# Optimization experiments

Measured on AMD Instinct MI355X. Metric: run time of the kernel, lower is better.

## Reference

```python
import jax, jax.numpy as jnp
import numpy as np

KS = 3          # deform conv kernel size
PAD = 1         # zero padding
NUM_HEADS = 6
DIM = 192


def conv2d(x, w, b=None, stride=1, padding=0):
    out = jax.lax.conv_general_dilated(
        x, w, (stride, stride), [(padding, padding), (padding, padding)],
        dimension_numbers=('NCHW', 'OIHW', 'NCHW'))
    if b is not None:
        out = out + b[None, :, None, None]
    return out


def deform_conv(x, p_conv_w, p_conv_b, dconv_w):
    B, C, H, W = x.shape
    N = KS * KS
    offset = conv2d(x, p_conv_w, p_conv_b, padding=1)           # [B, 2N, H, W]
    xp = jnp.pad(x, ((0, 0), (0, 0), (PAD, PAD), (PAD, PAD)))   # zero pad
    Hp, Wp = H + 2 * PAD, W + 2 * PAD
    # kernel-relative offsets p_n, row-major, first N are x (rows), last N are y (cols)
    r = jnp.arange(-(KS - 1) // 2, (KS - 1) // 2 + 1, dtype=x.dtype)
    pnx, pny = jnp.meshgrid(r, r, indexing='ij')
    p_n = jnp.concatenate([pnx.ravel(), pny.ravel()])           # [2N]
    # base grid p_0 (coords in padded image, starting at 1)
    p0x, p0y = jnp.meshgrid(jnp.arange(1, H + 1, dtype=x.dtype),
                            jnp.arange(1, W + 1, dtype=x.dtype), indexing='ij')
    p0 = jnp.concatenate([jnp.tile(p0x[None], (N, 1, 1)),
                          jnp.tile(p0y[None], (N, 1, 1))], axis=0)  # [2N,H,W]
    p = p0[None] + p_n[None, :, None, None] + offset            # [B,2N,H,W]
    p = jnp.transpose(p, (0, 2, 3, 1))                          # [B,H,W,2N]
    px, py = p[..., :N], p[..., N:]
    fx = jnp.floor(jax.lax.stop_gradient(px))                   # .detach().floor()
    fy = jnp.floor(jax.lax.stop_gradient(py))
    qx0 = jnp.clip(fx, 0, Hp - 1).astype(jnp.int32)
    qy0 = jnp.clip(fy, 0, Wp - 1).astype(jnp.int32)
    qx1 = jnp.clip(fx + 1, 0, Hp - 1).astype(jnp.int32)
    qy1 = jnp.clip(fy + 1, 0, Wp - 1).astype(jnp.int32)
    pxc = jnp.clip(px, 0, Hp - 1)
    pyc = jnp.clip(py, 0, Wp - 1)
    g_lt = (1 + (qx0 - pxc)) * (1 + (qy0 - pyc))
    g_rb = (1 - (qx1 - pxc)) * (1 - (qy1 - pyc))
    g_lb = (1 + (qx0 - pxc)) * (1 - (qy1 - pyc))
    g_rt = (1 - (qx1 - pxc)) * (1 + (qy0 - pyc))
    xf = xp.reshape(B, C, Hp * Wp)

    def gather(qx, qy):
        idx = (qx * Wp + qy).reshape(B, 1, -1)                  # [B,1,H*W*N]
        return jnp.take_along_axis(xf, idx, axis=-1).reshape(B, C, H, W, N)

    x_off = (g_lt[:, None] * gather(qx0, qy0)
             + g_rb[:, None] * gather(qx1, qy1)
             + g_lb[:, None] * gather(qx0, qy1)
             + g_rt[:, None] * gather(qx1, qy0))                # [B,C,H,W,N]
    # _reshape_x_offset: out[h*ks+r, w*ks+c] = x_off[h,w,r*ks+c]
    x_big = x_off.reshape(B, C, H, W, KS, KS)
    x_big = jnp.transpose(x_big, (0, 1, 2, 4, 3, 5)).reshape(B, C, H * KS, W * KS)
    return conv2d(x_big, dconv_w, stride=KS)                    # [B,C,H,W], no bias


def _l2_normalize(t):
    n = jnp.sqrt(jnp.sum(t * t, axis=-1, keepdims=True))
    return t / jnp.maximum(n, 1e-12)


def setup_inputs() -> dict:
    key = jax.random.key(0)
    ks = jax.random.split(key, 6)
    B, C, H, W = 2, DIM, 96, 96
    return {
        'x': jax.random.normal(ks[0], (B, C, H, W), dtype=jnp.float32),
        'p_conv_w': jax.random.normal(ks[1], (2 * KS * KS, C, 3, 3), dtype=jnp.float32) * 0.01,
        'p_conv_b': jax.random.normal(ks[2], (2 * KS * KS,), dtype=jnp.float32) * 0.01,
        'dconv_w': jax.random.normal(ks[3], (C, C, KS, KS), dtype=jnp.float32) * 0.02,
        'qkv_w': jax.random.normal(ks[4], (3 * C, C), dtype=jnp.float32) * 0.05,
        'proj_w': jax.random.normal(ks[5], (C, C), dtype=jnp.float32) * 0.05,
        'temperature': jnp.ones((NUM_HEADS, 1, 1), dtype=jnp.float32),
    }


def reference(x, p_conv_w, p_conv_b, dconv_w, qkv_w, proj_w, temperature):
    B, C, H, W = x.shape
    q = deform_conv(x, p_conv_w, p_conv_b, dconv_w)             # [B,C,H,W]
    qkv = jnp.einsum('bchw,oc->bohw', x, qkv_w)                 # 1x1 conv, no bias
    k, v = qkv[:, C:2 * C], qkv[:, 2 * C:]                      # q from qkv discarded
    hd = C // NUM_HEADS
    qh = _l2_normalize(q.reshape(B, NUM_HEADS, hd, H * W))
    kh = _l2_normalize(k.reshape(B, NUM_HEADS, hd, H * W))
    vh = v.reshape(B, NUM_HEADS, hd, H * W)
    attn = jnp.einsum('bhcn,bhdn->bhcd', qh, kh) * temperature[None]
    attn = jax.nn.softmax(attn, axis=-1)
    out = jnp.einsum('bhcd,bhdn->bhcn', attn, vh).reshape(B, C, H, W)
    return jnp.einsum('bchw,oc->bohw', out, proj_w)             # 1x1 project_out
```

## Files before the change

### kernel.cpp

```cpp
#include <hip/hip_runtime.h>

constexpr int SPLITS = 24;
constexpr size_t OFF_OFS  = 0;
constexpr size_t Q_OFS    = 331776;
constexpr size_t K_OFS    = Q_OFS + 3538944;
constexpr size_t V_OFS    = K_OFS + 3538944;
constexpr size_t NQ_OFS   = V_OFS + 3538944;
constexpr size_t NK_OFS   = NQ_OFS + 384;
constexpr size_t PART_OFS = NK_OFS + 384;
constexpr size_t ATTN_OFS = PART_OFS + (size_t)SPLITS * 12 * 1024;
constexpr size_t W2_OFS   = ATTN_OFS + 12288;
constexpr size_t XOFF_OFS = 11330304;
constexpr size_t WBT_OFS  = XOFF_OFS + 7962624;

typedef __attribute__((ext_vector_type(8))) short bf16x8;
typedef __attribute__((ext_vector_type(4))) float f32x4;

__device__ __forceinline__ unsigned bf16rne(float f) {
  unsigned u = __float_as_uint(f);
  return (u + 0x7fffu + ((u >> 16) & 1u)) >> 16;
}

__global__ __launch_bounds__(192) void k_offc_part(
    const float* __restrict__ x, const float* __restrict__ pw,
    float* __restrict__ part)
{
  __shared__ float band[16 * 4 * 98];
  int blk = blockIdx.x;
  int csp = blk % 12;
  int rem = blk / 12;
  int b  = rem / 48;
  int r0 = (rem % 48) * 2;
  int c0 = csp * 16;
  int t  = threadIdx.x;
  int r = t / 96, w = t % 96;

  for (int i = 0; i < 33; ++i) {
    int e = t + i * 192;
    if (e < 6272) {
      int cc = e / 392, r2 = e % 392;
      int row = r2 / 98, col = r2 % 98;
      int gr = r0 + row - 1, gc = col - 1;
      float v = 0.f;
      if (gr >= 0 && gr < 96 && gc >= 0 && gc < 96)
        v = x[((b * 192 + c0 + cc) * 96 + gr) * 96 + gc];
      band[cc * 392 + row * 98 + col] = v;
    }
  }
  __syncthreads();

  float acc[18] = {};
#pragma unroll 4
  for (int cc = 0; cc < 16; ++cc) {
    float bv[9];
#pragma unroll
    for (int ki = 0; ki < 3; ++ki)
#pragma unroll
      for (int kj = 0; kj < 3; ++kj)
        bv[ki * 3 + kj] = band[cc * 392 + (r + ki) * 98 + w + kj];
#pragma unroll
    for (int o = 0; o < 18; ++o) {
      float w9[9];
#pragma unroll
      for (int kk = 0; kk < 9; ++kk)
        w9[kk] = pw[(o * 192 + c0 + cc) * 9 + kk];
#pragma unroll
      for (int kk = 0; kk < 9; ++kk)
        acc[o] += w9[kk] * bv[kk];
    }
  }
  float* dst = &part[(size_t)csp * 663552 + ((size_t)(b * 18) * 96 + r0 + r) * 96 + w];
#pragma unroll
  for (int o = 0; o < 18; ++o)
    dst[(size_t)o * 9216] = acc[o];
}

__global__ __launch_bounds__(256) void k_offc_red(
    const float4* __restrict__ part4, const float* __restrict__ pb,
    float4* __restrict__ off4)
{
  int i4 = blockIdx.x * 256 + threadIdx.x;
  if (i4 >= 165888) return;
  int o = ((i4 * 4) / 9216) % 18;
  float bb = pb[o];
  float4 s = {bb, bb, bb, bb};
  for (int sp = 0; sp < 12; ++sp) {
    float4 v = part4[(size_t)sp * 165888 + i4];
    s.x += v.x; s.y += v.y; s.z += v.z; s.w += v.w;
  }
  off4[i4] = s;
}

__global__ __launch_bounds__(256) void k_cvtw(
    const float4* __restrict__ dw4, uint2* __restrict__ out, int n4)
{
  int i = blockIdx.x * 256 + threadIdx.x;
  if (i < n4) {
    float4 v = dw4[i];
    out[i] = uint2{bf16rne(v.x) | (bf16rne(v.y) << 16),
                   bf16rne(v.z) | (bf16rne(v.w) << 16)};
  }
}

__global__ __launch_bounds__(256) void k_sample(
    const float* __restrict__ x, const float* __restrict__ off,
    unsigned* __restrict__ xoffu, int b)
{
  __shared__ float twt[4][288];
  __shared__ int   tof[4][288];
  int blk = blockIdx.x;
  int csp = blk & 3;
  int tile = blk >> 2;
  int h  = tile / 3;
  int w0 = (tile % 3) * 32;
  int t  = threadIdx.x;

  for (int e = t; e < 288; e += 256) {
    int n = e >> 5, pix = e & 31;
    int ki = n / 3, kj = n % 3;
    int w = w0 + pix;
    float ox = off[((b * 18 + n) * 96 + h) * 96 + w];
    float oy = off[((b * 18 + 9 + n) * 96 + h) * 96 + w];
    float px = (float)(h + ki) + ox;
    float py = (float)(w + kj) + oy;
    float fx = floorf(px), fy = floorf(py);
    int qx0 = max(0, min(97, (int)fx));
    int qx1 = max(0, min(97, (int)fx + 1));
    int qy0 = max(0, min(97, (int)fy));
    int qy1 = max(0, min(97, (int)fy + 1));
    float pxc = fminf(fmaxf(px, 0.f), 97.f);
    float pyc = fminf(fmaxf(py, 0.f), 97.f);
    float wx0 = 1.f + ((float)qx0 - pxc);
    float wx1 = 1.f - ((float)qx1 - pxc);
    float wy0 = 1.f + ((float)qy0 - pyc);
    float wy1 = 1.f - ((float)qy1 - pyc);
    int X0 = qx0 - 1, X1 = qx1 - 1, Y0 = qy0 - 1, Y1 = qy1 - 1;
    bool vX0 = (unsigned)X0 < 96u, vX1 = (unsigned)X1 < 96u;
    bool vY0 = (unsigned)Y0 < 96u, vY1 = (unsigned)Y1 < 96u;
    twt[0][e] = (vX0 && vY0) ? wx0 * wy0 : 0.f;
    tof[0][e] = (vX0 && vY0) ? X0 * 96 + Y0 : 0;
    twt[1][e] = (vX1 && vY1) ? wx1 * wy1 : 0.f;
    tof[1][e] = (vX1 && vY1) ? X1 * 96 + Y1 : 0;
    twt[2][e] = (vX0 && vY1) ? wx0 * wy1 : 0.f;
    tof[2][e] = (vX0 && vY1) ? X0 * 96 + Y1 : 0;
    twt[3][e] = (vX1 && vY0) ? wx1 * wy0 : 0.f;
    tof[3][e] = (vX1 && vY0) ? X1 * 96 + Y0 : 0;
  }
  __syncthreads();

  int px = t & 31, cg = t >> 5;
  int c0 = csp * 48 + cg * 6;
  const float* bas = x + (size_t)(b * 192 + c0) * 9216;
  unsigned pixg = (unsigned)(h * 96 + w0 + px);
  for (int cp = 0; cp < 3; ++cp) {
    float vv[2][9];
#pragma unroll
    for (int n = 0; n < 9; ++n) {
      int e2 = n * 32 + px;
      float wlt = twt[0][e2], wrb = twt[1][e2], wlb = twt[2][e2], wrt = twt[3][e2];
      int olt = tof[0][e2], orb = tof[1][e2], olb = tof[2][e2], ort = tof[3][e2];
      const float* b0 = bas + cp * 2 * 9216;
      const float* b1 = b0 + 9216;
      vv[0][n] = wlt * b0[olt] + wrb * b0[orb] + wlb * b0[olb] + wrt * b0[ort];
      vv[1][n] = wlt * b1[olt] + wrb * b1[orb] + wlb * b1[olb] + wrt * b1[ort];
    }
    unsigned baseDW = (pixg * 1728u + (unsigned)(c0 + cp * 2) * 9u) >> 1;
#pragma unroll
    for (int jj = 0; jj < 9; ++jj) {
      constexpr int idx0[9] = {0,0,0,0,0,1,1,1,1};
      constexpr int idx1[9] = {0,0,0,0,1,1,1,1,1};
      xoffu[baseDW + jj] = bf16rne(vv[idx0[jj]][(2 * jj) % 9])
                         | (bf16rne(vv[idx1[jj]][(2 * jj + 1) % 9]) << 16);
    }
  }
}

__global__ __launch_bounds__(64) void k_dgemm(
    const unsigned short* __restrict__ xofft, const unsigned short* __restrict__ wbt,
    float* __restrict__ q, int b)
{
  int blk = blockIdx.x;
  int og = blk & 3;
  int pt = blk >> 2;
  int l  = threadIdx.x;
  int lo = l & 15, hi = l >> 4;
  const char* X = (const char*)xofft;
  const char* W = (const char*)wbt;
  size_t a0 = ((size_t)(og * 48 + lo)      * 1728 + hi * 8) * 2;
  size_t a1 = ((size_t)(og * 48 + 16 + lo) * 1728 + hi * 8) * 2;
  size_t a2 = ((size_t)(og * 48 + 32 + lo) * 1728 + hi * 8) * 2;
  size_t b0 = ((size_t)(pt * 32 + lo)      * 1728 + hi * 8) * 2;
  size_t b1 = ((size_t)(pt * 32 + 16 + lo) * 1728 + hi * 8) * 2;
  f32x4 acc00 = {}, acc01 = {}, acc10 = {}, acc11 = {}, acc20 = {}, acc21 = {};
#pragma unroll 2
  for (int k0 = 0; k0 < 3456; k0 += 64) {
    bf16x8 av0 = *(const bf16x8*)(W + a0 + k0);
    bf16x8 av1 = *(const bf16x8*)(W + a1 + k0);
    bf16x8 av2 = *(const bf16x8*)(W + a2 + k0);
    bf16x8 bv0 = *(const bf16x8*)(X + b0 + k0);
    bf16x8 bv1 = *(const bf16x8*)(X + b1 + k0);
    acc00 = __builtin_amdgcn_mfma_f32_16x16x32_bf16(av0, bv0, acc00, 0, 0, 0);
    acc01 = __builtin_amdgcn_mfma_f32_16x16x32_bf16(av0, bv1, acc01, 0, 0, 0);
    acc10 = __builtin_amdgcn_mfma_f32_16x16x32_bf16(av1, bv0, acc10, 0, 0, 0);
    acc11 = __builtin_amdgcn_mfma_f32_16x16x32_bf16(av1, bv1, acc11, 0, 0, 0);
    acc20 = __builtin_amdgcn_mfma_f32_16x16x32_bf16(av2, bv0, acc20, 0, 0, 0);
    acc21 = __builtin_amdgcn_mfma_f32_16x16x32_bf16(av2, bv1, acc21, 0, 0, 0);
  }
  f32x4* accs[3][2] = {{&acc00, &acc01}, {&acc10, &acc11}, {&acc20, &acc21}};
#pragma unroll
  for (int fo = 0; fo < 3; ++fo)
#pragma unroll
    for (int fp = 0; fp < 2; ++fp)
#pragma unroll
      for (int r = 0; r < 4; ++r)
        q[(size_t)(b * 192 + og * 48 + fo * 16 + hi * 4 + r) * 9216
          + pt * 32 + fp * 16 + lo] = (*accs[fo][fp])[r];
}

__global__ __launch_bounds__(384) void k_qkv(
    const float* __restrict__ x, const float* __restrict__ qkvw,
    float* __restrict__ kbuf, float* __restrict__ vbuf)
{
  __shared__ __align__(16) float Al[16 * 388];
  __shared__ __align__(16) float Bl[16 * 32];
  int blk = blockIdx.x;
  int b = blk / 288;
  int pix0 = (blk % 288) * 32;
  int t = threadIdx.x;
  int og = t >> 3, pg = t & 7;
  float acc[8][4] = {};
  float ra[16], rb2[2];
#pragma unroll
  for (int i = 0; i < 16; ++i) {
    int e = t + i * 384;
    ra[i] = qkvw[(size_t)(192 + (e >> 4)) * 192 + (e & 15)];
  }
#pragma unroll
  for (int i = 0; i < 2; ++i) {
    int e = t + i * 384;
    rb2[i] = (e < 512) ? x[(size_t)(b * 192 + (e >> 5)) * 9216 + pix0 + (e & 31)] : 0.f;
  }
  for (int c0 = 0; c0 < 192; c0 += 16) {
#pragma unroll
    for (int i = 0; i < 16; ++i) {
      int e = t + i * 384;
      Al[(e & 15) * 388 + (e >> 4)] = ra[i];
    }
#pragma unroll
    for (int i = 0; i < 2; ++i) {
      int e = t + i * 384;
      if (e < 512) Bl[e] = rb2[i];
    }
    __syncthreads();
    if (c0 + 16 < 192) {
#pragma unroll
      for (int i = 0; i < 16; ++i) {
        int e = t + i * 384;
        ra[i] = qkvw[(size_t)(192 + (e >> 4)) * 192 + c0 + 16 + (e & 15)];
      }
#pragma unroll
      for (int i = 0; i < 2; ++i) {
        int e = t + i * 384;
        rb2[i] = (e < 512) ? x[(size_t)(b * 192 + c0 + 16 + (e >> 5)) * 9216 + pix0 + (e & 31)] : 0.f;
      }
    }
    const float4* B4 = (const float4*)Bl;
    const float4* A4 = (const float4*)Al;
#pragma unroll
    for (int k = 0; k < 16; ++k) {
      float4 bv = B4[k * 8 + pg];
      float4 va0 = A4[k * 97 + og * 2];
      float4 va1 = A4[k * 97 + og * 2 + 1];
      float av[8] = {va0.x, va0.y, va0.z, va0.w, va1.x, va1.y, va1.z, va1.w};
#pragma unroll
      for (int i = 0; i < 8; ++i) {
        acc[i][0] += av[i] * bv.x; acc[i][1] += av[i] * bv.y;
        acc[i][2] += av[i] * bv.z; acc[i][3] += av[i] * bv.w;
      }
    }
    __syncthreads();
  }
#pragma unroll
  for (int i = 0; i < 8; ++i) {
    int o = og * 8 + i;
    float* dst = (o < 192) ? &kbuf[(size_t)(b * 192 + o) * 9216]
                           : &vbuf[(size_t)(b * 192 + o - 192) * 9216];
    *(float4*)(dst + pix0 + pg * 4) = {acc[i][0], acc[i][1], acc[i][2], acc[i][3]};
  }
}

__global__ __launch_bounds__(256) void k_norms(
    const float* __restrict__ qbuf, const float* __restrict__ kbuf,
    float* __restrict__ nq, float* __restrict__ nk)
{
  __shared__ float red[4];
  int blk = blockIdx.x;
  int which = blk / 384, r = blk % 384;
  const float* src = (which ? kbuf : qbuf) + (size_t)r * 9216;
  int t = threadIdx.x;
  float s = 0.f;
  const float4* s4 = (const float4*)src;
  for (int i = t; i < 2304; i += 256) {
    float4 v = s4[i];
    s += v.x * v.x + v.y * v.y + v.z * v.z + v.w * v.w;
  }
#pragma unroll
  for (int o = 32; o; o >>= 1) s += __shfl_xor(s, o);
  if ((t & 63) == 0) red[t >> 6] = s;
  __syncthreads();
  if (t == 0) {
    float tot = red[0] + red[1] + red[2] + red[3];
    (which ? nk : nq)[r] = 1.f / fmaxf(sqrtf(tot), 1e-12f);
  }
}

__global__ __launch_bounds__(256) void k_gram(
    const float* __restrict__ qbuf, const float* __restrict__ kbuf,
    float* __restrict__ part)
{
  __shared__ float sq[32 * 65], sk[32 * 65];
  int blk = blockIdx.x;
  int split = blk / 12, r = blk % 12;
  int b = r / 6, hh = r % 6;
  int n0 = split * 384;
  int t = threadIdx.x;
  int c = t >> 3, dg = t & 7;
  float acc[4] = {};
  for (int sc = 0; sc < 6; ++sc) {
    __syncthreads();
    for (int i = t; i < 2048; i += 256) {
      int cc = i >> 6, j = i & 63;
      size_t g = (size_t)(b * 192 + hh * 32 + cc) * 9216 + n0 + sc * 64 + j;
      sq[cc * 65 + j] = qbuf[g];
      sk[cc * 65 + j] = kbuf[g];
    }
    __syncthreads();
#pragma unroll 8
    for (int j = 0; j < 64; ++j) {
      float qv = sq[c * 65 + j];
#pragma unroll
      for (int i2 = 0; i2 < 4; ++i2)
        acc[i2] += qv * sk[(dg * 4 + i2) * 65 + j];
    }
  }
  float* dst = &part[((size_t)split * 12 + b * 6 + hh) * 1024 + c * 32 + dg * 4];
  *(float4*)dst = {acc[0], acc[1], acc[2], acc[3]};
}

__global__ __launch_bounds__(1024) void k_softmax(
    const float* __restrict__ part, const float* __restrict__ nq,
    const float* __restrict__ nk, const float* __restrict__ temp,
    float* __restrict__ attn)
{
  int bi = blockIdx.x;
  int b = bi / 6, h = bi % 6;
  int t = threadIdx.x;
  int c = t >> 5, d = t & 31;
  float val = 0.f;
  for (int s = 0; s < SPLITS; ++s) val += part[((size_t)s * 12 + bi) * 1024 + t];
  val *= nq[b * 192 + h * 32 + c] * nk[b * 192 + h * 32 + d] * temp[h];
  float m = val;
#pragma unroll
  for (int o = 16; o; o >>= 1) m = fmaxf(m, __shfl_xor(m, o));
  float e = expf(val - m);
  float s = e;
#pragma unroll
  for (int o = 16; o; o >>= 1) s += __shfl_xor(s, o);
  attn[(size_t)bi * 1024 + t] = e / s;
}

__global__ __launch_bounds__(256) void k_w2(
    const float* __restrict__ attn, const float* __restrict__ projw,
    float* __restrict__ w2)
{
  __shared__ float sa[32 * 33];
  int bi = blockIdx.x;
  int b = bi / 6, h = bi % 6;
  int t = threadIdx.x;
  for (int i = t; i < 1024; i += 256)
    sa[(i >> 5) * 33 + (i & 31)] = attn[(size_t)bi * 1024 + i];
  __syncthreads();
  for (int e = t; e < 6144; e += 256) {
    int o = e >> 5, d = e & 31;
    float s = 0.f;
#pragma unroll 8
    for (int ci = 0; ci < 32; ++ci)
      s += projw[o * 192 + h * 32 + ci] * sa[ci * 33 + d];
    w2[((size_t)b * 192 + o) * 192 + h * 32 + d] = s;
  }
}

__global__ __launch_bounds__(384) void k_out(
    const float* __restrict__ vbuf, const float* __restrict__ w2,
    float* __restrict__ out)
{
  __shared__ __align__(16) float Al[16 * 196];
  __shared__ __align__(16) float Bl[16 * 32];
  int blk = blockIdx.x;
  int b = blk / 288;
  int pix0 = (blk % 288) * 32;
  int t = threadIdx.x;
  int og = t >> 3, pg = t & 7;
  float acc[4][4] = {};
  float ra[8], rb2[2];
#pragma unroll
  for (int i = 0; i < 8; ++i) {
    int e = t + i * 384;
    ra[i] = w2[(size_t)(b * 192 + (e >> 4)) * 192 + (e & 15)];
  }
#pragma unroll
  for (int i = 0; i < 2; ++i) {
    int e = t + i * 384;
    rb2[i] = (e < 512) ? vbuf[(size_t)(b * 192 + (e >> 5)) * 9216 + pix0 + (e & 31)] : 0.f;
  }
  for (int c0 = 0; c0 < 192; c0 += 16) {
#pragma unroll
    for (int i = 0; i < 8; ++i) {
      int e = t + i * 384;
      Al[(e & 15) * 196 + (e >> 4)] = ra[i];
    }
#pragma unroll
    for (int i = 0; i < 2; ++i) {
      int e = t + i * 384;
      if (e < 512) Bl[e] = rb2[i];
    }
    __syncthreads();
    if (c0 + 16 < 192) {
#pragma unroll
      for (int i = 0; i < 8; ++i) {
        int e = t + i * 384;
        ra[i] = w2[(size_t)(b * 192 + (e >> 4)) * 192 + c0 + 16 + (e & 15)];
      }
#pragma unroll
      for (int i = 0; i < 2; ++i) {
        int e = t + i * 384;
        rb2[i] = (e < 512) ? vbuf[(size_t)(b * 192 + c0 + 16 + (e >> 5)) * 9216 + pix0 + (e & 31)] : 0.f;
      }
    }
    const float4* B4 = (const float4*)Bl;
    const float4* A4 = (const float4*)Al;
#pragma unroll
    for (int k = 0; k < 16; ++k) {
      float4 bv = B4[k * 8 + pg];
      float4 va = A4[k * 49 + og];
      float av[4] = {va.x, va.y, va.z, va.w};
#pragma unroll
      for (int i = 0; i < 4; ++i) {
        acc[i][0] += av[i] * bv.x; acc[i][1] += av[i] * bv.y;
        acc[i][2] += av[i] * bv.z; acc[i][3] += av[i] * bv.w;
      }
    }
    __syncthreads();
  }
#pragma unroll
  for (int i = 0; i < 4; ++i) {
    int o = og * 4 + i;
    *(float4*)&out[(size_t)(b * 192 + o) * 9216 + pix0 + pg * 4]
        = {acc[i][0], acc[i][1], acc[i][2], acc[i][3]};
  }
}

extern "C" void kernel_launch(void* const* d_in, const int* in_sizes, int n_in,
                              void* d_out, int out_size, void* d_ws, size_t ws_size,
                              hipStream_t stream) {
  (void)in_sizes; (void)n_in; (void)out_size; (void)ws_size;
  const float* x     = (const float*)d_in[0];
  const float* pw    = (const float*)d_in[1];
  const float* pb    = (const float*)d_in[2];
  const float* dw    = (const float*)d_in[3];
  const float* qkvw  = (const float*)d_in[4];
  const float* projw = (const float*)d_in[5];
  const float* temp  = (const float*)d_in[6];
  float* ws   = (float*)d_ws;
  float* off  = ws + OFF_OFS;
  float* qb   = ws + Q_OFS;
  float* kb   = ws + K_OFS;
  float* vb   = ws + V_OFS;
  float* nq   = ws + NQ_OFS;
  float* nk   = ws + NK_OFS;
  float* part = ws + PART_OFS;
  float* attn = ws + ATTN_OFS;
  float* w2   = ws + W2_OFS;
  float* opart = ws + XOFF_OFS;
  unsigned*       xoffu = (unsigned*)(ws + XOFF_OFS);
  unsigned short* xofft = (unsigned short*)xoffu;
  unsigned short* wbt   = (unsigned short*)(ws + WBT_OFS);
  float* out  = (float*)d_out;

  k_offc_part  <<<dim3(1152), dim3(192), 0, stream>>>(x, pw, opart);
  k_offc_red   <<<dim3(648),  dim3(256), 0, stream>>>((const float4*)opart, pb, (float4*)off);
  k_cvtw       <<<dim3(324),  dim3(256), 0, stream>>>((const float4*)dw, (uint2*)wbt, 82944);
  k_qkv        <<<dim3(576),  dim3(384), 0, stream>>>(x, qkvw, kb, vb);
  for (int b = 0; b < 2; ++b) {
    k_sample   <<<dim3(1152), dim3(256), 0, stream>>>(x, off, xoffu, b);
    k_dgemm    <<<dim3(1152), dim3(64),  0, stream>>>(xofft, wbt, qb, b);
  }
  k_norms      <<<dim3(768),  dim3(256), 0, stream>>>(qb, kb, nq, nk);
  k_gram       <<<dim3(288),  dim3(256), 0, stream>>>(qb, kb, part);
  k_softmax    <<<dim3(12),   dim3(1024),0, stream>>>(part, nq, nk, temp, attn);
  k_w2         <<<dim3(12),   dim3(256), 0, stream>>>(attn, projw, w2);
  k_out        <<<dim3(576),  dim3(384), 0, stream>>>(vb, w2, out);
}
```

Before: 482.0 us.

## Move qkv projection and gram matrix to bf16 MFMA with bf16 q/k storage

Replaces the fp32 FMA qkv 1x1 conv with a bf16 MFMA kernel that converts x tiles to bf16 in LDS and uses a pre-converted bf16 weight copy. The q and k intermediates are now stored in bf16, which halves their memory traffic for the norm and gram kernels. The gram is reworked as an MFMA kernel with more splits. This cuts fp32 ALU work and bandwidth, at the cost of bf16 rounding on q, k and the x inputs to the projection, plus an extra weight-conversion launch.

```diff
diff --git a/kernel.cpp b/kernel.cpp
--- a/kernel.cpp
+++ b/kernel.cpp
@@ -1,9 +1,12 @@
 #include <hip/hip_runtime.h>
 
 constexpr int SPLITS = 24;
+constexpr int GSPL   = 48;
 constexpr size_t OFF_OFS  = 0;
 constexpr size_t Q_OFS    = 331776;
+constexpr size_t QKVWBF_OFS = Q_OFS + 1769472;
 constexpr size_t K_OFS    = Q_OFS + 3538944;
+constexpr size_t PART2_OFS = K_OFS + 1769472;
 constexpr size_t V_OFS    = K_OFS + 3538944;
 constexpr size_t NQ_OFS   = V_OFS + 3538944;
 constexpr size_t NK_OFS   = NQ_OFS + 384;
@@ -19,6 +22,9 @@
 __device__ __forceinline__ unsigned bf16rne(float f) {
   unsigned u = __float_as_uint(f);
   return (u + 0x7fffu + ((u >> 16) & 1u)) >> 16;
+}
+__device__ __forceinline__ float bf2f(unsigned hw) {
+  return __uint_as_float(hw << 16);
 }
 
 __global__ __launch_bounds__(192) void k_offc_part(
@@ -100,6 +106,74 @@
     out[i] = uint2{bf16rne(v.x) | (bf16rne(v.y) << 16),
                    bf16rne(v.z) | (bf16rne(v.w) << 16)};
   }
+}
+__global__ __launch_bounds__(256) void k_cvtqkvw(
+    const float* __restrict__ qkvw, unsigned* __restrict__ wqu)
+{
+  int i = blockIdx.x * 256 + threadIdx.x;
+  if (i < 36864)
+    wqu[i] = bf16rne(qkvw[36864 + 2 * i]) | (bf16rne(qkvw[36864 + 2 * i + 1]) << 16);
+}
+
+__global__ __launch_bounds__(64) void k_qkv_mfma(
+    const float* __restrict__ x, const unsigned short* __restrict__ wq,
+    unsigned short* __restrict__ kbf, float* __restrict__ vbuf)
+{
+  __shared__ unsigned Bl[32 * 100];
+  int id = blockIdx.x;
+  int b  = id / 2304;
+  int rem = id % 2304;
+  int og = rem & 7;
+  int pt = rem >> 3;
+  int pix0 = pt * 32;
+  int l = threadIdx.x;
+  int lo = l & 15, hi = l >> 4;
+
+  const float* xb = x + (size_t)b * 192 * 9216 + pix0;
+  for (int i = 0; i < 48; ++i) {
+    int e = l + i * 64;
+    int cp = e >> 5, px = e & 31;
+    float x0 = xb[(size_t)(2 * cp) * 9216 + px];
+    float x1 = xb[(size_t)(2 * cp + 1) * 9216 + px];
+    Bl[px * 100 + cp] = bf16rne(x0) | (bf16rne(x1) << 16);
+  }
+  __syncthreads();
+
+  const unsigned short* A0 = wq + (og * 48 + lo) * 192 + hi * 8;
+  const unsigned short* A1 = A0 + 16 * 192;
+  const unsigned short* A2 = A0 + 32 * 192;
+  const unsigned* B0 = &Bl[lo * 100 + hi * 4];
+  const unsigned* B1 = &Bl[(16 + lo) * 100 + hi * 4];
+  f32x4 acc00 = {}, acc01 = {}, acc10 = {}, acc11 = {}, acc20 = {}, acc21 = {};
+#pragma unroll
+  for (int ks = 0; ks < 6; ++ks) {
+    bf16x8 av0 = *(const bf16x8*)(A0 + ks * 32);
+    bf16x8 av1 = *(const bf16x8*)(A1 + ks * 32);
+    bf16x8 av2 = *(const bf16x8*)(A2 + ks * 32);
+    bf16x8 bv0 = *(const bf16x8*)(B0 + ks * 16);
+    bf16x8 bv1 = *(const bf16x8*)(B1 + ks * 16);
+    acc00 = __builtin_amdgcn_mfma_f32_16x16x32_bf16(av0, bv0, acc00, 0, 0, 0);
+    acc01 = __builtin_amdgcn_mfma_f32_16x16x32_bf16(av0, bv1, acc01, 0, 0, 0);
+    acc10 = __builtin_amdgcn_mfma_f32_16x16x32_bf16(av1, bv0, acc10, 0, 0, 0);
+    acc11 = __builtin_amdgcn_mfma_f32_16x16x32_bf16(av1, bv1, acc11, 0, 0, 0);
+    acc20 = __builtin_amdgcn_mfma_f32_16x16x32_bf16(av2, bv0, acc20, 0, 0, 0);
+    acc21 = __builtin_amdgcn_mfma_f32_16x16x32_bf16(av2, bv1, acc21, 0, 0, 0);
+  }
+  f32x4* accs[3][2] = {{&acc00, &acc01}, {&acc10, &acc11}, {&acc20, &acc21}};
+#pragma unroll
+  for (int fo = 0; fo < 3; ++fo)
+#pragma unroll
+    for (int fp = 0; fp < 2; ++fp)
+#pragma unroll
+      for (int r = 0; r < 4; ++r) {
+        int o = og * 48 + fo * 16 + hi * 4 + r;
+        int px = pix0 + fp * 16 + lo;
+        float vv = (*accs[fo][fp])[r];
+        if (o < 192)
+          kbf[(size_t)(b * 192 + o) * 9216 + px] = (unsigned short)bf16rne(vv);
+        else
+          vbuf[(size_t)(b * 192 + (o - 192)) * 9216 + px] = vv;
+      }
 }
 
 __global__ __launch_bounds__(256) void k_sample(
@@ -177,7 +251,7 @@
 
 __global__ __launch_bounds__(64) void k_dgemm(
     const unsigned short* __restrict__ xofft, const unsigned short* __restrict__ wbt,
-    float* __restrict__ q, int b)
+    unsigned short* __restrict__ qbf, int b)
 {
   int blk = blockIdx.x;
   int og = blk & 3;
@@ -213,96 +287,29 @@
     for (int fp = 0; fp < 2; ++fp)
 #pragma unroll
       for (int r = 0; r < 4; ++r)
-        q[(size_t)(b * 192 + og * 48 + fo * 16 + hi * 4 + r) * 9216
-          + pt * 32 + fp * 16 + lo] = (*accs[fo][fp])[r];
-}
-
-__global__ __launch_bounds__(384) void k_qkv(
-    const float* __restrict__ x, const float* __restrict__ qkvw,
-    float* __restrict__ kbuf, float* __restrict__ vbuf)
-{
-  __shared__ __align__(16) float Al[16 * 388];
-  __shared__ __align__(16) float Bl[16 * 32];
-  int blk = blockIdx.x;
-  int b = blk / 288;
-  int pix0 = (blk % 288) * 32;
-  int t = threadIdx.x;
-  int og = t >> 3, pg = t & 7;
-  float acc[8][4] = {};
-  float ra[16], rb2[2];
-#pragma unroll
-  for (int i = 0; i < 16; ++i) {
-    int e = t + i * 384;
-    ra[i] = qkvw[(size_t)(192 + (e >> 4)) * 192 + (e & 15)];
-  }
-#pragma unroll
-  for (int i = 0; i < 2; ++i) {
-    int e = t + i * 384;
-    rb2[i] = (e < 512) ? x[(size_t)(b * 192 + (e >> 5)) * 9216 + pix0 + (e & 31)] : 0.f;
-  }
-  for (int c0 = 0; c0 < 192; c0 += 16) {
-#pragma unroll
-    for (int i = 0; i < 16; ++i) {
-      int e = t + i * 384;
-      Al[(e & 15) * 388 + (e >> 4)] = ra[i];
-    }
-#pragma unroll
-    for (int i = 0; i < 2; ++i) {
-      int e = t + i * 384;
-      if (e < 512) Bl[e] = rb2[i];
-    }
-    __syncthreads();
-    if (c0 + 16 < 192) {
-#pragma unroll
-      for (int i = 0; i < 16; ++i) {
-        int e = t + i * 384;
-        ra[i] = qkvw[(size_t)(192 + (e >> 4)) * 192 + c0 + 16 + (e & 15)];
-      }
-#pragma unroll
-      for (int i = 0; i < 2; ++i) {
-        int e = t + i * 384;
-        rb2[i] = (e < 512) ? x[(size_t)(b * 192 + c0 + 16 + (e >> 5)) * 9216 + pix0 + (e & 31)] : 0.f;
-      }
-    }
-    const float4* B4 = (const float4*)Bl;
-    const float4* A4 = (const float4*)Al;
-#pragma unroll
-    for (int k = 0; k < 16; ++k) {
-      float4 bv = B4[k * 8 + pg];
-      float4 va0 = A4[k * 97 + og * 2];
-      float4 va1 = A4[k * 97 + og * 2 + 1];
-      float av[8] = {va0.x, va0.y, va0.z, va0.w, va1.x, va1.y, va1.z, va1.w};
-#pragma unroll
-      for (int i = 0; i < 8; ++i) {
-        acc[i][0] += av[i] * bv.x; acc[i][1] += av[i] * bv.y;
-        acc[i][2] += av[i] * bv.z; acc[i][3] += av[i] * bv.w;
-      }
-    }
-    __syncthreads();
-  }
-#pragma unroll
-  for (int i = 0; i < 8; ++i) {
-    int o = og * 8 + i;
-    float* dst = (o < 192) ? &kbuf[(size_t)(b * 192 + o) * 9216]
-                           : &vbuf[(size_t)(b * 192 + o - 192) * 9216];
-    *(float4*)(dst + pix0 + pg * 4) = {acc[i][0], acc[i][1], acc[i][2], acc[i][3]};
-  }
+        qbf[(size_t)(b * 192 + og * 48 + fo * 16 + hi * 4 + r) * 9216
+            + pt * 32 + fp * 16 + lo] = (unsigned short)bf16rne((*accs[fo][fp])[r]);
 }
 
 __global__ __launch_bounds__(256) void k_norms(
-    const float* __restrict__ qbuf, const float* __restrict__ kbuf,
+    const unsigned short* __restrict__ qbf, const unsigned short* __restrict__ kbf,
     float* __restrict__ nq, float* __restrict__ nk)
 {
   __shared__ float red[4];
   int blk = blockIdx.x;
   int which = blk / 384, r = blk % 384;
-  const float* src = (which ? kbuf : qbuf) + (size_t)r * 9216;
+  const uint4* s4 = (const uint4*)((which ? kbf : qbf) + (size_t)r * 9216);
   int t = threadIdx.x;
   float s = 0.f;
-  const float4* s4 = (const float4*)src;
-  for (int i = t; i < 2304; i += 256) {
-    float4 v = s4[i];
-    s += v.x * v.x + v.y * v.y + v.z * v.z + v.w * v.w;
+  for (int i = t; i < 1152; i += 256) {
+    uint4 v = s4[i];
+    unsigned ws_[4] = {v.x, v.y, v.z, v.w};
+#pragma unroll
+    for (int j = 0; j < 4; ++j) {
+      float a = bf2f(ws_[j] & 0xffffu);
+      float bq = __uint_as_float(ws_[j] & 0xffff0000u);
+      s += a * a + bq * bq;
+    }
   }
 #pragma unroll
   for (int o = 32; o; o >>= 1) s += __shfl_xor(s, o);
@@ -314,41 +321,45 @@
   }
 }
 
-__global__ __launch_bounds__(256) void k_gram(
-    const float* __restrict__ qbuf, const float* __restrict__ kbuf,
-    float* __restrict__ part)
-{
-  __shared__ float sq[32 * 65], sk[32 * 65];
+__global__ __launch_bounds__(64) void k_gram_mfma(
+    const unsigned short* __restrict__ qbf, const unsigned short* __restrict__ kbf,
+    float* __restrict__ part2)
+{
   int blk = blockIdx.x;
   int split = blk / 12, r = blk % 12;
   int b = r / 6, hh = r % 6;
-  int n0 = split * 384;
-  int t = threadIdx.x;
-  int c = t >> 3, dg = t & 7;
-  float acc[4] = {};
-  for (int sc = 0; sc < 6; ++sc) {
-    __syncthreads();
-    for (int i = t; i < 2048; i += 256) {
-      int cc = i >> 6, j = i & 63;
-      size_t g = (size_t)(b * 192 + hh * 32 + cc) * 9216 + n0 + sc * 64 + j;
-      sq[cc * 65 + j] = qbuf[g];
-      sk[cc * 65 + j] = kbuf[g];
-    }
-    __syncthreads();
-#pragma unroll 8
-    for (int j = 0; j < 64; ++j) {
-      float qv = sq[c * 65 + j];
-#pragma unroll
-      for (int i2 = 0; i2 < 4; ++i2)
-        acc[i2] += qv * sk[(dg * 4 + i2) * 65 + j];
-    }
-  }
-  float* dst = &part[((size_t)split * 12 + b * 6 + hh) * 1024 + c * 32 + dg * 4];
-  *(float4*)dst = {acc[0], acc[1], acc[2], acc[3]};
+  int n0 = split * 192;
+  int l = threadIdx.x;
+  int lo = l & 15, hi = l >> 4;
+  const unsigned short* Q0 = qbf + (size_t)(b * 192 + hh * 32 + lo) * 9216 + n0 + hi * 8;
+  const unsigned short* Q1 = Q0 + (size_t)16 * 9216;
+  const unsigned short* K0 = kbf + (size_t)(b * 192 + hh * 32 + lo) * 9216 + n0 + hi * 8;
+  const unsigned short* K1 = K0 + (size_t)16 * 9216;
+  f32x4 g00 = {}, g01 = {}, g10 = {}, g11 = {};
+#pragma unroll
+  for (int ks = 0; ks < 6; ++ks) {
+    bf16x8 qa0 = *(const bf16x8*)(Q0 + ks * 32);
+    bf16x8 qa1 = *(const bf16x8*)(Q1 + ks * 32);
+    bf16x8 kb0 = *(const bf16x8*)(K0 + ks * 32);
+    bf16x8 kb1 = *(const bf16x8*)(K1 + ks * 32);
+    g00 = __builtin_amdgcn_mfma_f32_16x16x32_bf16(qa0, kb0, g00, 0, 0, 0);
+    g01 = __builtin_amdgcn_mfma_f32_16x16x32_bf16(qa0, kb1, g01, 0, 0, 0);
+    g10 = __builtin_amdgcn_mfma_f32_16x16x32_bf16(qa1, kb0, g10, 0, 0, 0);
+    g11 = __builtin_amdgcn_mfma_f32_16x16x32_bf16(qa1, kb1, g11, 0, 0, 0);
+  }
+  float* dst = part2 + ((size_t)split * 12 + r) * 1024;
+  f32x4* gs[2][2] = {{&g00, &g01}, {&g10, &g11}};
+#pragma unroll
+  for (int fc = 0; fc < 2; ++fc)
+#pragma unroll
+    for (int fd = 0; fd < 2; ++fd)
+#pragma unroll
+      for (int rr = 0; rr < 4; ++rr)
+        dst[(fc * 16 + hi * 4 + rr) * 32 + fd * 16 + lo] = (*gs[fc][fd])[rr];
 }
 
 __global__ __launch_bounds__(1024) void k_softmax(
-    const float* __restrict__ part, const float* __restrict__ nq,
+    const float* __restrict__ part2, const float* __restrict__ nq,
     const float* __restrict__ nk, const float* __restrict__ temp,
     float* __restrict__ attn)
 {
@@ -357,7 +368,7 @@
   int t = threadIdx.x;
   int c = t >> 5, d = t & 31;
   float val = 0.f;
-  for (int s = 0; s < SPLITS; ++s) val += part[((size_t)s * 12 + bi) * 1024 + t];
+  for (int s = 0; s < GSPL; ++s) val += part2[((size_t)s * 12 + bi) * 1024 + t];
   val *= nq[b * 192 + h * 32 + c] * nk[b * 192 + h * 32 + d] * temp[h];
   float m = val;
 #pragma unroll
@@ -473,12 +484,14 @@
   const float* temp  = (const float*)d_in[6];
   float* ws   = (float*)d_ws;
   float* off  = ws + OFF_OFS;
-  float* qb   = ws + Q_OFS;
-  float* kb   = ws + K_OFS;
+  unsigned short* qbf = (unsigned short*)(ws + Q_OFS);
+  unsigned*       wqu = (unsigned*)(ws + QKVWBF_OFS);
+  unsigned short* wq  = (unsigned short*)wqu;
+  unsigned short* kbf = (unsigned short*)(ws + K_OFS);
+  float* part2 = ws + PART2_OFS;
   float* vb   = ws + V_OFS;
   float* nq   = ws + NQ_OFS;
   float* nk   = ws + NK_OFS;
-  float* part = ws + PART_OFS;
   float* attn = ws + ATTN_OFS;
   float* w2   = ws + W2_OFS;
   float* opart = ws + XOFF_OFS;
@@ -490,14 +503,15 @@
   k_offc_part  <<<dim3(1152), dim3(192), 0, stream>>>(x, pw, opart);
   k_offc_red   <<<dim3(648),  dim3(256), 0, stream>>>((const float4*)opart, pb, (float4*)off);
   k_cvtw       <<<dim3(324),  dim3(256), 0, stream>>>((const float4*)dw, (uint2*)wbt, 82944);
-  k_qkv        <<<dim3(576),  dim3(384), 0, stream>>>(x, qkvw, kb, vb);
+  k_cvtqkvw    <<<dim3(144),  dim3(256), 0, stream>>>(qkvw, wqu);
+  k_qkv_mfma   <<<dim3(4608), dim3(64),  0, stream>>>(x, wq, kbf, vb);
   for (int b = 0; b < 2; ++b) {
     k_sample   <<<dim3(1152), dim3(256), 0, stream>>>(x, off, xoffu, b);
-    k_dgemm    <<<dim3(1152), dim3(64),  0, stream>>>(xofft, wbt, qb, b);
-  }
-  k_norms      <<<dim3(768),  dim3(256), 0, stream>>>(qb, kb, nq, nk);
-  k_gram       <<<dim3(288),  dim3(256), 0, stream>>>(qb, kb, part);
-  k_softmax    <<<dim3(12),   dim3(1024),0, stream>>>(part, nq, nk, temp, attn);
+    k_dgemm    <<<dim3(1152), dim3(64),  0, stream>>>(xofft, wbt, qbf, b);
+  }
+  k_norms      <<<dim3(768),  dim3(256), 0, stream>>>(qbf, kbf, nq, nk);
+  k_gram_mfma  <<<dim3(576),  dim3(64),  0, stream>>>(qbf, kbf, part2);
+  k_softmax    <<<dim3(12),   dim3(1024),0, stream>>>(part2, nq, nk, temp, attn);
   k_w2         <<<dim3(12),   dim3(256), 0, stream>>>(attn, projw, w2);
   k_out        <<<dim3(576),  dim3(384), 0, stream>>>(vb, w2, out);
 }
```

Result: faster. 413.0 us (-14.3%).
